# Kernel optimization log

Measured on AMD Instinct MI355X. Metric: run time of the kernel, lower is better.

## Reference

```python
import jax, jax.numpy as jnp
import numpy as np

B, N, P, PL = 8, 16, 128, 16
D, DS, DTR, DFF, EL = 128, 16, 8, 256, 2


def setup_inputs() -> dict:
    key = jax.random.key(0)
    ks = jax.random.split(key, 16)
    g = lambda i, shape, s=0.02: jax.random.normal(ks[i], shape, dtype=jnp.float32) * s
    A_init = jnp.broadcast_to(jnp.log(jnp.arange(1, DS + 1, dtype=jnp.float32)), (EL, 2, D, DS))
    return dict(
        x=jax.random.normal(ks[0], (B, N, P, PL), dtype=jnp.float32),
        view=jax.random.normal(ks[1], (B, 1, D), dtype=jnp.float32),
        wp_w=g(2, (D, PL)), wp_b=jnp.zeros((D,), jnp.float32),
        m_in_w=g(3, (EL, 2, 2 * D, D)),
        m_conv_w=g(4, (EL, 2, D, 2), 0.5), m_conv_b=jnp.zeros((EL, 2, D), jnp.float32),
        m_xproj_w=g(5, (EL, 2, DTR + 2 * DS, D)),
        m_dt_w=g(6, (EL, 2, D, DTR), 0.1), m_dt_b=jnp.full((EL, 2, D), -4.6, jnp.float32),
        m_Alog=jnp.array(A_init),
        m_D=jnp.ones((EL, 2, D), jnp.float32),
        m_out_w=g(7, (EL, 2, D, D)),
        ffn_w1=g(8, (EL, DFF, D)), ffn_b1=jnp.zeros((EL, DFF), jnp.float32),
        ffn_w2=g(9, (EL, D, DFF)), ffn_b2=jnp.zeros((EL, D), jnp.float32),
        ln1_g=jnp.ones((EL, D), jnp.float32), ln1_b=jnp.zeros((EL, D), jnp.float32),
        ln2_g=jnp.ones((EL, D), jnp.float32), ln2_b=jnp.zeros((EL, D), jnp.float32),
        lnf_g=jnp.ones((D,), jnp.float32), lnf_b=jnp.zeros((D,), jnp.float32),
    )


def _ln(x, g, b, eps=1e-5):
    m = x.mean(-1, keepdims=True)
    v = x.var(-1, keepdims=True)
    return (x - m) * jax.lax.rsqrt(v + eps) * g + b


def _mamba(u, in_w, conv_w, conv_b, xproj_w, dt_w, dt_b, A_log, Dp, out_w):
    # u: [b, L, d]; d_inner == d_model (expand=1), causal depthwise conv with kernel 2
    dtr, ds = dt_w.shape[1], A_log.shape[1]
    xz = u @ in_w.T                               # [b, L, 2d]
    xc, z = jnp.split(xz, 2, axis=-1)
    xp = jnp.pad(xc, ((0, 0), (1, 0), (0, 0)))    # left-pad (d_conv-1 = 1)
    xc = xp[:, :-1, :] * conv_w[:, 0] + xp[:, 1:, :] * conv_w[:, 1] + conv_b
    xc = jax.nn.silu(xc)
    dbc = xc @ xproj_w.T                          # [b, L, dtr + 2*ds]
    dt = jax.nn.softplus(dbc[..., :dtr] @ dt_w.T + dt_b)   # [b, L, d]
    Bm = dbc[..., dtr:dtr + ds]                   # [b, L, n]
    Cm = dbc[..., dtr + ds:]                      # [b, L, n]
    A = -jnp.exp(A_log)                           # [d, n]
    dA = jnp.exp(dt[..., None] * A)               # [b, L, d, n]
    dBx = dt[..., None] * Bm[:, :, None, :] * xc[..., None]  # [b, L, d, n]

    def step(h, ab):
        a, bx = ab
        h = a * h + bx
        return h, h

    h0 = jnp.zeros((u.shape[0], dt.shape[-1], ds), u.dtype)
    _, hs = jax.lax.scan(step, h0, (jnp.moveaxis(dA, 1, 0), jnp.moveaxis(dBx, 1, 0)))
    y = jnp.einsum('lbdn,bln->bld', hs, Cm)       # [b, L, d]
    y = y + xc * Dp
    y = y * jax.nn.silu(z)
    return y @ out_w.T


def _layer(u, pf, pr, w1, b1, w2, b2, g1, be1, g2, be2):
    fwd = _mamba(u, *pf)
    rev = _mamba(u[:, ::-1], *pr)[:, ::-1]
    u = u + fwd + rev
    xr = _ln(u, g1, be1)
    y = jax.nn.relu(xr @ w1.T + b1) @ w2.T + b2   # 1x1 conv FFN == pointwise linear
    return _ln(xr + y, g2, be2)


def reference(x, view, wp_w, wp_b, m_in_w, m_conv_w, m_conv_b, m_xproj_w, m_dt_w,
              m_dt_b, m_Alog, m_D, m_out_w, ffn_w1, ffn_b1, ffn_w2, ffn_b2,
              ln1_g, ln1_b, ln2_g, ln2_b, lnf_g, lnf_b):
    b, n, p, _ = x.shape
    u = x @ wp_w.T + wp_b                         # [b, n, p, d]
    d = u.shape[-1]
    u = u.reshape(b, n * p, d)
    u = jnp.concatenate([u, view], axis=1)        # [b, n*p+1, d]
    for l in range(m_in_w.shape[0]):
        pf = (m_in_w[l, 0], m_conv_w[l, 0], m_conv_b[l, 0], m_xproj_w[l, 0],
              m_dt_w[l, 0], m_dt_b[l, 0], m_Alog[l, 0], m_D[l, 0], m_out_w[l, 0])
        pr = (m_in_w[l, 1], m_conv_w[l, 1], m_conv_b[l, 1], m_xproj_w[l, 1],
              m_dt_w[l, 1], m_dt_b[l, 1], m_Alog[l, 1], m_D[l, 1], m_out_w[l, 1])
        u = _layer(u, pf, pr, ffn_w1[l], ffn_b1[l], ffn_w2[l], ffn_b2[l],
                   ln1_g[l], ln1_b[l], ln2_g[l], ln2_b[l])
    u = _ln(u, lnf_g, lnf_b)
    z = u[:, :-1, :].reshape(b, n, p, d)
    return z.transpose(0, 1, 3, 2)                # [b, n, d, p]
```

## Files before the change

### kernel.cpp

```cpp
#include <hip/hip_runtime.h>
#include <hip/hip_bf16.h>
#include <math.h>

#define DEV __device__ __forceinline__

constexpr int B  = 8,  N = 16, P = 128, PL = 16;
constexpr int D  = 128, DS = 16, DTR = 8, DFF = 256, EL = 2;
constexpr int L  = N * P + 1;
constexpr int BL = B * L;
constexpr int CT = 32;
constexpr int NC = (L + CT - 1) / CT;
constexpr int MT128 = (BL + 127) / 128;
constexpr int MT64  = (BL + 63) / 64;
constexpr int KS = 136;
constexpr int HS = 264;

using bf16x8 = __attribute__((ext_vector_type(8))) __bf16;
using f32x4  = __attribute__((ext_vector_type(4))) float;

DEV float sigmoidf_(float x) { return 1.0f / (1.0f + __expf(-x)); }

DEV float wsum(float v) {
#pragma unroll
  for (int m = 32; m; m >>= 1) v += __shfl_xor(v, m, 64);
  return v;
}

DEV void pow_tree(float r, float* pw) {
  float r2 = r * r;
  float r3 = r2 * r;
  float r4 = r2 * r2;
  float r8 = r4 * r4;
  float r12 = r8 * r4;
  pw[0] = r;       pw[1] = r2;      pw[2] = r3;      pw[3] = r4;
  pw[4] = r4 * r;  pw[5] = r4 * r2; pw[6] = r4 * r3; pw[7] = r8;
  pw[8] = r8 * r;  pw[9] = r8 * r2; pw[10] = r8 * r3; pw[11] = r12;
  pw[12] = r12 * r; pw[13] = r12 * r2; pw[14] = r12 * r3; pw[15] = r12 * r4;
}

DEV bool an_is_linear(const float* An) {
  bool ok = true;
#pragma unroll
  for (int n = 0; n < DS; ++n)
    ok = ok && (fabsf(An[n] + (float)(n + 1)) < 1e-3f * (n + 1));
  return ok;
}

__global__ __launch_bounds__(256) void k_prep(
    const float* __restrict__ in_w, const float* __restrict__ conv_w,
    const float* __restrict__ xproj, const float* __restrict__ out_w,
    const float* __restrict__ w1, const float* __restrict__ w2,
    __bf16* __restrict__ weff, __bf16* __restrict__ xpw_bf,
    __bf16* __restrict__ outw_bf, __bf16* __restrict__ w1_bf,
    __bf16* __restrict__ w2_bf)
{
  int g = blockIdx.x * 256 + threadIdx.x;
  if (g < 262144) {
    int l = g >> 17;
    int r = g & 131071;
    int dir = r >> 16;
    int r2 = r & 65535;
    int col = r2 >> 8;
    int kk = r2 & 255;
    int chunk = kk >> 7, k = kk & 127;
    int ld = l * 2 + dir;
    float v;
    if (col < 128) {
      v = in_w[((size_t)ld * 256 + col) * 128 + k] *
          conv_w[((size_t)ld * 128 + col) * 2 + chunk];
    } else {
      v = chunk ? in_w[((size_t)ld * 256 + col) * 128 + k] : 0.f;
    }
    weff[((size_t)ld * 256 + col) * 256 + chunk * 128 + k] = (__bf16)v;
    return;
  }
  g -= 262144;
  if (g < 20480) { xpw_bf[g] = (__bf16)xproj[g]; return; }
  g -= 20480;
  if (g < 65536) {
    int k = g & 127; int q = g >> 7; int n = q & 127; int q2 = q >> 7;
    int dir = q2 & 1; int l = q2 >> 1;
    outw_bf[((size_t)(l * 128 + n)) * 256 + dir * 128 + k] = (__bf16)out_w[g];
    return;
  }
  g -= 65536;
  if (g < 65536) { w1_bf[g] = (__bf16)w1[g]; return; }
  g -= 65536;
  if (g < 65536) { w2_bf[g] = (__bf16)w2[g]; return; }
}

__global__ __launch_bounds__(256) void k_embed(
    const float* __restrict__ x, const float* __restrict__ view,
    const float* __restrict__ wp_w, const float* __restrict__ wp_b,
    float* __restrict__ U, __bf16* __restrict__ Ubf)
{
  int g = blockIdx.x * 256 + threadIdx.x;
  if (g >= BL * D) return;
  int d = g & (D - 1);
  int row = g >> 7;
  int b = row / L, t = row % L;
  float acc;
  if (t < N * P) {
    const float* xr = x + ((size_t)b * N * P + t) * PL;
    acc = wp_b[d];
#pragma unroll
    for (int k = 0; k < PL; ++k) acc += xr[k] * wp_w[d * PL + k];
  } else {
    acc = view[b * D + d];
  }
  U[(size_t)row * D + d] = acc;
  Ubf[(size_t)row * D + d] = (__bf16)acc;
}

__global__ __launch_bounds__(256) void k_front(
    const __bf16* __restrict__ Ubf, const __bf16* __restrict__ Weff,
    const float* __restrict__ conv_b_l, const __bf16* __restrict__ xpw,
    const float* __restrict__ dt_w_l, const float* __restrict__ dt_b_l,
    __bf16* __restrict__ XCCbf, __bf16* __restrict__ Zbf,
    float* __restrict__ BCb, __bf16* __restrict__ DTbf)
{
  __shared__ short As[64 * KS];
  __shared__ short Ws[64 * KS];
  __shared__ float dbs[64][9];
  int bx = blockIdx.x;
  int rdir = bx / MT64;
  int tile = bx % MT64;
  bool isx = (blockIdx.y == 0);
  int tid = threadIdx.x;
  int m0 = tile * 64;
  const __bf16* Wb = Weff + (size_t)rdir * 256 * 256;
  int wave = tid >> 6, lane = tid & 63, lm = lane & 15, lq = lane >> 4;
  int rr0 = tid >> 4, gcol = tid & 15;

  int aoff[4];
  unsigned vmask = 0, smask = 0;
  int shif = rdir ? 128 : -128;
#pragma unroll
  for (int i = 0; i < 4; ++i) {
    int rr = rr0 + 16 * i;
    int m = m0 + rr;
    aoff[i] = 0;
    if (m < BL) {
      int b = m / L, s = m - b * L;
      int idx1 = rdir ? (L - 1 - s) : s;
      aoff[i] = (b * L + idx1) * 128 + gcol * 8;
      vmask |= 1u << i;
      if (s >= 1) smask |= 1u << i;
    }
  }

  f32x4 zero4 = {0.f, 0.f, 0.f, 0.f};
  f32x4 acc[8];
#pragma unroll
  for (int c = 0; c < 8; ++c) acc[c] = zero4;

  int kc0 = isx ? 0 : 1;
  int colx = isx ? 0 : 128;
  for (int kc = kc0; kc < 2; ++kc) {
    if (kc != kc0) __syncthreads();
#pragma unroll
    for (int i = 0; i < 4; ++i) {
      int rr = rr0 + 16 * i;
      int4 v = make_int4(0, 0, 0, 0);
      bool ok = (vmask >> i) & 1;
      if (kc == 0) ok = ok && ((smask >> i) & 1);
      if (ok) v = *(const int4*)(Ubf + aoff[i] + (kc == 0 ? shif : 0));
      *(int4*)&As[rr * KS + gcol * 8] = v;
    }
    for (int ch = 0; ch < 2; ++ch) {
      if (ch) __syncthreads();
#pragma unroll
      for (int i = 0; i < 4; ++i) {
        int rr = rr0 + 16 * i;
        int4 v = *(const int4*)(Wb + (size_t)(colx + ch * 64 + rr) * 256 + kc * 128 + gcol * 8);
        *(int4*)&Ws[rr * KS + gcol * 8] = v;
      }
      __syncthreads();
      for (int ks = 0; ks < 128; ks += 32) {
        bf16x8 af = *(const bf16x8*)&As[(wave * 16 + lm) * KS + ks + lq * 8];
#pragma unroll
        for (int c = 0; c < 4; ++c) {
          bf16x8 bfr = *(const bf16x8*)&Ws[(c * 16 + lm) * KS + ks + lq * 8];
          acc[ch * 4 + c] = __builtin_amdgcn_mfma_f32_16x16x32_bf16(af, bfr, acc[ch * 4 + c], 0, 0, 0);
        }
      }
    }
  }

  if (!isx) {
#pragma unroll
    for (int cg = 0; cg < 8; ++cg) {
      int col = cg * 16 + lm;
#pragma unroll
      for (int e = 0; e < 4; ++e) {
        int m = m0 + wave * 16 + lq * 4 + e;
        if (m < BL)
          Zbf[((size_t)rdir * BL + m) * 128 + col] = (__bf16)acc[cg][e];
      }
    }
    return;
  }

  __syncthreads();
#pragma unroll
  for (int cg = 0; cg < 8; ++cg) {
    int col = cg * 16 + lm;
    float cb = conv_b_l[rdir * 128 + col];
#pragma unroll
    for (int e = 0; e < 4; ++e) {
      int rl = wave * 16 + lq * 4 + e;
      int m = m0 + rl;
      float v = acc[cg][e] + cb;
      float o = v * sigmoidf_(v);
      __bf16 ob = (__bf16)o;
      if (m < BL) XCCbf[((size_t)rdir * BL + m) * 128 + col] = ob;
      As[rl * KS + col] = (short)__builtin_bit_cast(unsigned short, ob);
    }
  }
#pragma unroll
  for (int i = 0; i < 3; ++i) {
    int rr = rr0 + 16 * i;
    int4 v = make_int4(0, 0, 0, 0);
    if (rr < 40) v = *(const int4*)(xpw + ((size_t)rdir * 40 + rr) * 128 + gcol * 8);
    *(int4*)&Ws[rr * KS + gcol * 8] = v;
  }
  __syncthreads();
  f32x4 acc2[3];
#pragma unroll
  for (int c = 0; c < 3; ++c) acc2[c] = zero4;
  for (int ks = 0; ks < 128; ks += 32) {
    bf16x8 af = *(const bf16x8*)&As[(wave * 16 + lm) * KS + ks + lq * 8];
#pragma unroll
    for (int c = 0; c < 3; ++c) {
      bf16x8 bfr = *(const bf16x8*)&Ws[(c * 16 + lm) * KS + ks + lq * 8];
      acc2[c] = __builtin_amdgcn_mfma_f32_16x16x32_bf16(af, bfr, acc2[c], 0, 0, 0);
    }
  }
#pragma unroll
  for (int c = 0; c < 3; ++c) {
    int col = c * 16 + lm;
#pragma unroll
    for (int e = 0; e < 4; ++e) {
      int rl = wave * 16 + lq * 4 + e;
      int m = m0 + rl;
      float v = acc2[c][e];
      if (col < DTR) dbs[rl][col] = v;
      else if (col < DTR + 2 * DS && m < BL)
        BCb[((size_t)rdir * BL + m) * 32 + (col - DTR)] = v;
    }
  }
  __syncthreads();
  {
    int dloc = tid & 127;
    int rpar = tid >> 7;
    const float* dw = dt_w_l + ((size_t)rdir * 128 + dloc) * 8;
    float dwr[8];
#pragma unroll
    for (int j = 0; j < 8; ++j) dwr[j] = dw[j];
    float db = dt_b_l[rdir * 128 + dloc];
    for (int rr = rpar; rr < 64; rr += 2) {
      int m = m0 + rr;
      if (m >= BL) break;
      float a = db;
#pragma unroll
      for (int j = 0; j < 8; ++j) a = fmaf(dbs[rr][j], dwr[j], a);
      float dtv = (a > 20.f) ? a : log1pf(__expf(a));
      DTbf[((size_t)rdir * BL + m) * 128 + dloc] = (__bf16)dtv;
    }
  }
}

__global__ __launch_bounds__(128) void k_scanA(
    const __bf16* __restrict__ DTbf, const __bf16* __restrict__ XCCbf,
    const float* __restrict__ BCb, const float* __restrict__ Alog_l,
    float* __restrict__ HC, float* __restrict__ DTS)
{
  __shared__ float Bs[CT][DS];
  __shared__ __bf16 DTs[CT][128];
  __shared__ __bf16 XCs[CT][128];
  __shared__ float HT[128][DS + 1];
  int blk = blockIdx.x;
  int c  = blk % NC;
  int rb = blk / NC;
  int rdir = rb / B;
  int d = threadIdx.x;
  int s0 = c * CT;
  int cn = min(CT, L - s0);
  size_t rowbase = (size_t)rb * L + s0;
  for (int q = d; q < cn * DS; q += 128)
    Bs[q >> 4][q & 15] = BCb[(rowbase + (q >> 4)) * 32 + (q & 15)];
  for (int q = d; q < cn * 16; q += 128) {
    int row = q >> 4, c8 = (q & 15) * 8;
    *(int4*)&DTs[row][c8] = *(const int4*)(DTbf + (rowbase + row) * D + c8);
    *(int4*)&XCs[row][c8] = *(const int4*)(XCCbf + (rowbase + row) * D + c8);
  }
  float An[DS];
  const float* Ab = Alog_l + (size_t)rdir * D * DS + (size_t)d * DS;
#pragma unroll
  for (int n = 0; n < DS; ++n) An[n] = -__expf(Ab[n]);
  bool fast = an_is_linear(An);
  __syncthreads();
  float h[DS];
#pragma unroll
  for (int n = 0; n < DS; ++n) h[n] = 0.f;
  float dts = 0.f;
  if (fast) {
    for (int ss = 0; ss < cn; ++ss) {
      float dt = (float)DTs[ss][d];
      float xc = (float)XCs[ss][d];
      dts += dt;
      float e = dt * xc;
      float pw[DS];
      pow_tree(__expf(-dt), pw);
#pragma unroll
      for (int n = 0; n < DS; ++n)
        h[n] = fmaf(pw[n], h[n], e * Bs[ss][n]);
    }
  } else {
    for (int ss = 0; ss < cn; ++ss) {
      float dt = (float)DTs[ss][d];
      float xc = (float)XCs[ss][d];
      dts += dt;
      float e = dt * xc;
#pragma unroll
      for (int n = 0; n < DS; ++n)
        h[n] = __expf(dt * An[n]) * h[n] + e * Bs[ss][n];
    }
  }
  DTS[(size_t)blk * D + d] = dts;
#pragma unroll
  for (int n = 0; n < DS; ++n) HT[d][n] = h[n];
  __syncthreads();
  for (int q = d; q < D * DS; q += 128) {
    int n = q >> 7, dd = q & 127;
    HC[((size_t)blk * DS + n) * D + dd] = HT[dd][n];
  }
}

__global__ __launch_bounds__(128) void k_scanB(
    const float* __restrict__ HC, const float* __restrict__ DTS,
    const float* __restrict__ Alog_l, float* __restrict__ HIN)
{
  int rb = blockIdx.x >> 4;
  int n  = blockIdx.x & 15;
  int rdir = rb / B;
  int d = threadIdx.x;
  float An_v = -__expf(Alog_l[((size_t)rdir * D + d) * DS + n]);
  float hc[8], dts[8];
#pragma unroll
  for (int k = 0; k < 8; ++k) {
    int cc = (k < NC) ? k : NC - 1;
    hc[k]  = HC[((size_t)(rb * NC + cc) * DS + n) * D + d];
    dts[k] = DTS[((size_t)(rb * NC + cc)) * D + d];
  }
  float h = 0.f;
  for (int c = 0; c < NC; c += 8) {
#pragma unroll
    for (int k = 0; k < 8; ++k) {
      int cc = c + k;
      if (cc >= NC) break;
      HIN[((size_t)(rb * NC + cc) * DS + n) * D + d] = h;
      h = __expf(dts[k] * An_v) * h + hc[k];
      int cp = cc + 8 < NC ? cc + 8 : NC - 1;
      hc[k]  = HC[((size_t)(rb * NC + cp) * DS + n) * D + d];
      dts[k] = DTS[((size_t)(rb * NC + cp)) * D + d];
    }
  }
}

__global__ __launch_bounds__(128) void k_scanC(
    const __bf16* __restrict__ DTbf, const __bf16* __restrict__ XCCbf,
    const float* __restrict__ BCb, const __bf16* __restrict__ Zbf,
    const float* __restrict__ HIN, const float* __restrict__ Alog_l,
    const float* __restrict__ Dp_l, __bf16* __restrict__ YMbf)
{
  __shared__ float Bsm[CT][DS];
  __shared__ float Csm[CT][DS];
  __shared__ __bf16 DTs[CT][128];
  __shared__ __bf16 XCs[CT][128];
  __shared__ __bf16 Zs[CT][128];
  int blk = blockIdx.x;
  int c  = blk % NC;
  int rb = blk / NC;
  int rdir = rb / B;
  int b = rb % B;
  int d = threadIdx.x;
  int s0 = c * CT;
  int cn = min(CT, L - s0);
  size_t rowbase = (size_t)rb * L + s0;
  for (int q = d; q < cn * 2 * DS; q += 128) {
    int ss = q >> 5, j = q & 31;
    float vv = BCb[(rowbase + ss) * 32 + j];
    if (j < DS) Bsm[ss][j] = vv; else Csm[ss][j - DS] = vv;
  }
  for (int q = d; q < cn * 16; q += 128) {
    int row = q >> 4, c8 = (q & 15) * 8;
    *(int4*)&DTs[row][c8] = *(const int4*)(DTbf + (rowbase + row) * D + c8);
    *(int4*)&XCs[row][c8] = *(const int4*)(XCCbf + (rowbase + row) * D + c8);
    *(int4*)&Zs[row][c8]  = *(const int4*)(Zbf + (rowbase + row) * D + c8);
  }
  float An[DS];
  const float* Ab = Alog_l + (size_t)rdir * D * DS + (size_t)d * DS;
#pragma unroll
  for (int n = 0; n < DS; ++n) An[n] = -__expf(Ab[n]);
  bool fast = an_is_linear(An);
  float h[DS];
#pragma unroll
  for (int n = 0; n < DS; ++n)
    h[n] = HIN[((size_t)blk * DS + n) * D + d];
  float Dpv = Dp_l[rdir * D + d];
  __syncthreads();
  if (fast) {
    for (int ss = 0; ss < cn; ++ss) {
      float dt = (float)DTs[ss][d];
      float xc = (float)XCs[ss][d];
      float z  = (float)Zs[ss][d];
      float e = dt * xc;
      float pw[DS];
      pow_tree(__expf(-dt), pw);
      float y = xc * Dpv;
#pragma unroll
      for (int n = 0; n < DS; ++n) {
        h[n] = fmaf(pw[n], h[n], e * Bsm[ss][n]);
        y = fmaf(h[n], Csm[ss][n], y);
      }
      y *= z * sigmoidf_(z);
      int s = s0 + ss;
      int tt = rdir ? (L - 1 - s) : s;
      YMbf[((size_t)b * L + tt) * 256 + rdir * 128 + d] = (__bf16)y;
    }
  } else {
    for (int ss = 0; ss < cn; ++ss) {
      float dt = (float)DTs[ss][d];
      float xc = (float)XCs[ss][d];
      float z  = (float)Zs[ss][d];
      float e = dt * xc;
      float y = xc * Dpv;
#pragma unroll
      for (int n = 0; n < DS; ++n) {
        h[n] = __expf(dt * An[n]) * h[n] + e * Bsm[ss][n];
        y = fmaf(h[n], Csm[ss][n], y);
      }
      y *= z * sigmoidf_(z);
      int s = s0 + ss;
      int tt = rdir ? (L - 1 - s) : s;
      YMbf[((size_t)b * L + tt) * 256 + rdir * 128 + d] = (__bf16)y;
    }
  }
}

__global__ __launch_bounds__(256) void k_tail(
    const __bf16* __restrict__ YMbf, const __bf16* __restrict__ Wout,
    const float* __restrict__ g1, const float* __restrict__ be1,
    const __bf16* __restrict__ w1bf, const float* __restrict__ b1,
    const __bf16* __restrict__ w2bf, const float* __restrict__ b2,
    const float* __restrict__ g2, const float* __restrict__ be2,
    float* __restrict__ U, __bf16* __restrict__ Ubf,
    int last, const float* __restrict__ lnfg, const float* __restrict__ lnfb,
    float* __restrict__ outp)
{
  __shared__ short AX[64 * KS];
  __shared__ short BH[128 * KS];
  __shared__ short Ws[64 * KS];
  int m0 = blockIdx.x * 64;
  int tid = threadIdx.x;
  int wave = tid >> 6, lane = tid & 63, lm = lane & 15, lq = lane >> 4;
  int rr0 = tid >> 4, gcol = tid & 15;
  f32x4 zero4 = {0.f, 0.f, 0.f, 0.f};

  f32x4 acc[8];
#pragma unroll
  for (int c = 0; c < 8; ++c) acc[c] = zero4;
  for (int kc = 0; kc < 2; ++kc) {
    if (kc) __syncthreads();
    for (int q = tid; q < 64 * 16; q += 256) {
      int rr = q >> 4, g = q & 15;
      int m = m0 + rr;
      int4 v = make_int4(0, 0, 0, 0);
      if (m < BL) v = *(const int4*)(YMbf + (size_t)m * 256 + kc * 128 + g * 8);
      *(int4*)&AX[rr * KS + g * 8] = v;
    }
    for (int q = tid; q < 128 * 16; q += 256) {
      int rr = q >> 4, g = q & 15;
      int4 v = *(const int4*)(Wout + (size_t)rr * 256 + kc * 128 + g * 8);
      *(int4*)&BH[rr * KS + g * 8] = v;
    }
    __syncthreads();
    for (int ks = 0; ks < 128; ks += 32) {
      bf16x8 af = *(const bf16x8*)&AX[(wave * 16 + lm) * KS + ks + lq * 8];
#pragma unroll
      for (int c = 0; c < 8; ++c) {
        bf16x8 bfr = *(const bf16x8*)&BH[(c * 16 + lm) * KS + ks + lq * 8];
        acc[c] = __builtin_amdgcn_mfma_f32_16x16x32_bf16(af, bfr, acc[c], 0, 0, 0);
      }
    }
  }
  __syncthreads();

  {
    float g1c[8], be1c[8];
#pragma unroll
    for (int c = 0; c < 8; ++c) {
      int col = c * 16 + lm;
      g1c[c] = g1[col]; be1c[c] = be1[col];
    }
#pragma unroll
    for (int r = 0; r < 4; ++r) {
      int row = m0 + wave * 16 + lq * 4 + r;
      bool valid = row < BL;
      float os[8];
      float sum = 0.f;
#pragma unroll
      for (int c = 0; c < 8; ++c) {
        int col = c * 16 + lm;
        float uv = valid ? U[(size_t)row * 128 + col] : 0.f;
        os[c] = acc[c][r] + uv;
        sum += os[c];
      }
#pragma unroll
      for (int mm = 1; mm < 16; mm <<= 1) sum += __shfl_xor(sum, mm, 64);
      float mean = sum * (1.f / 128.f);
      float qv = 0.f;
#pragma unroll
      for (int c = 0; c < 8; ++c) { float dv = os[c] - mean; qv += dv * dv; }
#pragma unroll
      for (int mm = 1; mm < 16; mm <<= 1) qv += __shfl_xor(qv, mm, 64);
      float inv = rsqrtf(qv * (1.f / 128.f) + 1e-5f);
      int rl = wave * 16 + lq * 4 + r;
#pragma unroll
      for (int c = 0; c < 8; ++c) {
        int col = c * 16 + lm;
        float o = (os[c] - mean) * inv * g1c[c] + be1c[c];
        AX[rl * KS + col] = (short)__builtin_bit_cast(unsigned short, (__bf16)o);
      }
    }
  }

  for (int cc = 0; cc < 4; ++cc) {
    __syncthreads();
    for (int q = tid; q < 64 * 16; q += 256) {
      int rr = q >> 4, g = q & 15;
      int4 v = *(const int4*)(w1bf + (size_t)(cc * 64 + rr) * 128 + g * 8);
      *(int4*)&Ws[rr * KS + g * 8] = v;
    }
    __syncthreads();
    f32x4 a1[4];
#pragma unroll
    for (int c = 0; c < 4; ++c) a1[c] = zero4;
    for (int ks = 0; ks < 128; ks += 32) {
      bf16x8 af = *(const bf16x8*)&AX[(wave * 16 + lm) * KS + ks + lq * 8];
#pragma unroll
      for (int c = 0; c < 4; ++c) {
        bf16x8 bfr = *(const bf16x8*)&Ws[(c * 16 + lm) * KS + ks + lq * 8];
        a1[c] = __builtin_amdgcn_mfma_f32_16x16x32_bf16(af, bfr, a1[c], 0, 0, 0);
      }
    }
#pragma unroll
    for (int c = 0; c < 4; ++c) {
      int col = cc * 64 + c * 16 + lm;
      float bb = b1[col];
#pragma unroll
      for (int e = 0; e < 4; ++e) {
        int rl = wave * 16 + lq * 4 + e;
        float hv = fmaxf(a1[c][e] + bb, 0.f);
        BH[rl * HS + col] = (short)__builtin_bit_cast(unsigned short, (__bf16)hv);
      }
    }
  }

  f32x4 a2[2][4];
#pragma unroll
  for (int nc = 0; nc < 2; ++nc)
#pragma unroll
    for (int c = 0; c < 4; ++c) a2[nc][c] = zero4;
  for (int nc = 0; nc < 2; ++nc) {
    for (int kc = 0; kc < 2; ++kc) {
      __syncthreads();
      for (int q = tid; q < 64 * 16; q += 256) {
        int rr = q >> 4, g = q & 15;
        int4 v = *(const int4*)(w2bf + (size_t)(nc * 64 + rr) * 256 + kc * 128 + g * 8);
        *(int4*)&Ws[rr * KS + g * 8] = v;
      }
      __syncthreads();
      for (int ks = 0; ks < 128; ks += 32) {
        bf16x8 af = *(const bf16x8*)&BH[(wave * 16 + lm) * HS + kc * 128 + ks + lq * 8];
#pragma unroll
        for (int c = 0; c < 4; ++c) {
          bf16x8 bfr = *(const bf16x8*)&Ws[(c * 16 + lm) * KS + ks + lq * 8];
          a2[nc][c] = __builtin_amdgcn_mfma_f32_16x16x32_bf16(af, bfr, a2[nc][c], 0, 0, 0);
        }
      }
    }
  }
  {
    float b2c[8], g2c[8], be2c[8];
#pragma unroll
    for (int q = 0; q < 8; ++q) {
      int col = (q >> 2) * 64 + (q & 3) * 16 + lm;
      b2c[q] = b2[col]; g2c[q] = g2[col]; be2c[q] = be2[col];
    }
#pragma unroll
    for (int r = 0; r < 4; ++r) {
      int rl = wave * 16 + lq * 4 + r;
      int row = m0 + rl;
      bool valid = row < BL;
      float os[8];
      float sum = 0.f;
#pragma unroll
      for (int q = 0; q < 8; ++q) {
        int nc = q >> 2, c = q & 3;
        int col = nc * 64 + c * 16 + lm;
        __bf16 xb = __builtin_bit_cast(__bf16, (unsigned short)AX[rl * KS + col]);
        os[q] = a2[nc][c][r] + b2c[q] + (float)xb;
        sum += os[q];
      }
#pragma unroll
      for (int mm = 1; mm < 16; mm <<= 1) sum += __shfl_xor(sum, mm, 64);
      float mean = sum * (1.f / 128.f);
      float qv = 0.f;
#pragma unroll
      for (int q = 0; q < 8; ++q) { float dv = os[q] - mean; qv += dv * dv; }
#pragma unroll
      for (int mm = 1; mm < 16; mm <<= 1) qv += __shfl_xor(qv, mm, 64);
      float inv = rsqrtf(qv * (1.f / 128.f) + 1e-5f);
      float o[8];
#pragma unroll
      for (int q = 0; q < 8; ++q)
        o[q] = (os[q] - mean) * inv * g2c[q] + be2c[q];
      if (!last) {
        if (valid) {
#pragma unroll
          for (int q = 0; q < 8; ++q) {
            int col = (q >> 2) * 64 + (q & 3) * 16 + lm;
            U[(size_t)row * 128 + col] = o[q];
          }
        }
#pragma unroll
        for (int q = 0; q < 8; ++q) {
          int col = (q >> 2) * 64 + (q & 3) * 16 + lm;
          AX[rl * KS + col] = (short)__builtin_bit_cast(unsigned short, (__bf16)o[q]);
        }
      } else {
        float s2 = 0.f;
#pragma unroll
        for (int q = 0; q < 8; ++q) s2 += o[q];
#pragma unroll
        for (int mm = 1; mm < 16; mm <<= 1) s2 += __shfl_xor(s2, mm, 64);
        float mean2 = s2 * (1.f / 128.f);
        float qv2 = 0.f;
#pragma unroll
        for (int q = 0; q < 8; ++q) { float dv = o[q] - mean2; qv2 += dv * dv; }
#pragma unroll
        for (int mm = 1; mm < 16; mm <<= 1) qv2 += __shfl_xor(qv2, mm, 64);
        float inv2 = rsqrtf(qv2 * (1.f / 128.f) + 1e-5f);
        if (valid) {
          int bb = row / L;
          int t = row - bb * L;
          if (t < N * P) {
            int n = t >> 7, p = t & 127;
            size_t obase = (((size_t)bb * N + n) * D) * P + p;
#pragma unroll
            for (int q = 0; q < 8; ++q) {
              int col = (q >> 2) * 64 + (q & 3) * 16 + lm;
              float o2 = (o[q] - mean2) * inv2 * lnfg[col] + lnfb[col];
              outp[obase + (size_t)col * P] = o2;
            }
          }
        }
      }
    }
  }
  if (!last) {
    __syncthreads();
#pragma unroll
    for (int i = 0; i < 4; ++i) {
      int rr = rr0 + 16 * i;
      int m = m0 + rr;
      if (m < BL)
        *(int4*)(Ubf + (size_t)m * 128 + gcol * 8) = *(const int4*)&AX[rr * KS + gcol * 8];
    }
  }
}

extern "C" void kernel_launch(void* const* d_in, const int* in_sizes, int n_in,
                              void* d_out, int out_size, void* d_ws, size_t ws_size,
                              hipStream_t stream)
{
  (void)in_sizes; (void)n_in; (void)out_size; (void)ws_size;
  const float* x       = (const float*)d_in[0];
  const float* view    = (const float*)d_in[1];
  const float* wp_w    = (const float*)d_in[2];
  const float* wp_b    = (const float*)d_in[3];
  const float* m_in_w  = (const float*)d_in[4];
  const float* m_conv_w= (const float*)d_in[5];
  const float* m_conv_b= (const float*)d_in[6];
  const float* m_xproj = (const float*)d_in[7];
  const float* m_dt_w  = (const float*)d_in[8];
  const float* m_dt_b  = (const float*)d_in[9];
  const float* m_Alog  = (const float*)d_in[10];
  const float* m_Dp    = (const float*)d_in[11];
  const float* m_out_w = (const float*)d_in[12];
  const float* ffn_w1  = (const float*)d_in[13];
  const float* ffn_b1  = (const float*)d_in[14];
  const float* ffn_w2  = (const float*)d_in[15];
  const float* ffn_b2  = (const float*)d_in[16];
  const float* ln1_g   = (const float*)d_in[17];
  const float* ln1_b   = (const float*)d_in[18];
  const float* ln2_g   = (const float*)d_in[19];
  const float* ln2_b   = (const float*)d_in[20];
  const float* lnf_g   = (const float*)d_in[21];
  const float* lnf_b   = (const float*)d_in[22];
  float* out = (float*)d_out;

  float* W = (float*)d_ws;
  size_t off = 0;
  auto alloc = [&](size_t nfl) { float* p = W + off; off += (nfl + 3) & ~(size_t)3; return p; };
  float* U      = alloc((size_t)BL * D);
  float* Ubf_f  = alloc((size_t)BL * D / 2);
  float* XCC_f  = alloc((size_t)BL * D);
  float* Zbf_f  = alloc((size_t)BL * D);
  float* DT_f   = alloc((size_t)BL * D);
  float* BCb    = alloc((size_t)2 * BL * 2 * DS);
  float* YM_f   = alloc((size_t)BL * 256 / 2);
  float* HC     = alloc((size_t)2 * B * NC * D * DS);
  float* DTS    = alloc((size_t)2 * B * NC * D);
  float* HIN    = alloc((size_t)2 * B * NC * D * DS);
  float* weff_f = alloc(262144 / 2);
  float* xpw_f  = alloc(20480 / 2);
  float* outw_f = alloc(65536 / 2);
  float* w1_f   = alloc(65536 / 2);
  float* w2_f   = alloc(65536 / 2);

  __bf16* Ubf    = (__bf16*)Ubf_f;
  __bf16* XCCbf  = (__bf16*)XCC_f;
  __bf16* Zbf    = (__bf16*)Zbf_f;
  __bf16* DTbf   = (__bf16*)DT_f;
  __bf16* YMbf   = (__bf16*)YM_f;
  __bf16* weff   = (__bf16*)weff_f;
  __bf16* xpw_bf = (__bf16*)xpw_f;
  __bf16* outw_bf= (__bf16*)outw_f;
  __bf16* w1_bf  = (__bf16*)w1_f;
  __bf16* w2_bf  = (__bf16*)w2_f;

  k_prep<<<1872, 256, 0, stream>>>(m_in_w, m_conv_w, m_xproj, m_out_w, ffn_w1, ffn_w2,
                                   weff, xpw_bf, outw_bf, w1_bf, w2_bf);
  k_embed<<<(BL * D + 255) / 256, 256, 0, stream>>>(x, view, wp_w, wp_b, U, Ubf);

  for (int l = 0; l < EL; ++l) {
    const float* conv_b_l = m_conv_b + (size_t)l * 2 * D;
    const float* dt_w_l   = m_dt_w   + (size_t)l * 2 * D * DTR;
    const float* dt_b_l   = m_dt_b   + (size_t)l * 2 * D;
    const float* Alog_l   = m_Alog   + (size_t)l * 2 * D * DS;
    const float* Dp_l     = m_Dp     + (size_t)l * 2 * D;

    k_front <<<dim3(2 * MT64, 2), 256, 0, stream>>>(
        Ubf, weff + (size_t)l * 2 * 256 * 256, conv_b_l,
        xpw_bf + (size_t)l * 2 * 40 * 128, dt_w_l, dt_b_l,
        XCCbf, Zbf, BCb, DTbf);
    k_scanA <<<2 * B * NC, 128, 0, stream>>>(DTbf, XCCbf, BCb, Alog_l, HC, DTS);
    k_scanB <<<2 * B * 16, 128, 0, stream>>>(HC, DTS, Alog_l, HIN);
    k_scanC <<<2 * B * NC, 128, 0, stream>>>(DTbf, XCCbf, BCb, Zbf, HIN, Alog_l, Dp_l, YMbf);
    k_tail  <<<MT64, 256, 0, stream>>>(
        YMbf, outw_bf + (size_t)l * 128 * 256,
        ln1_g + l * D, ln1_b + l * D,
        w1_bf + (size_t)l * 256 * 128, ffn_b1 + l * DFF,
        w2_bf + (size_t)l * 128 * 256, ffn_b2 + l * D,
        ln2_g + l * D, ln2_b + l * D, U, Ubf,
        (l == EL - 1) ? 1 : 0, lnf_g, lnf_b, out);
  }
}
```

Baseline: 321.4 us.

## Halve k_tail row tile to 32 with 2x2 wave split and cross-wave LayerNorm

k_tail now processes 32 rows per block instead of 64, with the four waves arranged 2x2 so each wave owns 16 rows and half of the output columns. LayerNorm row statistics are combined across the two column-waves through a small shared-memory reduction buffer. Weight tiles are staged as full 128-row chunks, so there are fewer staging rounds per block. The grid doubles (about 514 blocks), which should fill more of the GPU's compute units, at the cost of more total weight reloads and extra barriers.

Measured after the change: 339.9 us. +5.8%, slower.

```diff
diff --git a/kernel.cpp b/kernel.cpp
--- a/kernel.cpp
+++ b/kernel.cpp
@@ -10,8 +10,8 @@
 constexpr int BL = B * L;
 constexpr int CT = 32;
 constexpr int NC = (L + CT - 1) / CT;
-constexpr int MT128 = (BL + 127) / 128;
 constexpr int MT64  = (BL + 63) / 64;
+constexpr int MT32  = (BL + 31) / 32;
 constexpr int KS = 136;
 constexpr int HS = 264;
 
@@ -19,12 +19,6 @@
 using f32x4  = __attribute__((ext_vector_type(4))) float;
 
 DEV float sigmoidf_(float x) { return 1.0f / (1.0f + __expf(-x)); }
-
-DEV float wsum(float v) {
-#pragma unroll
-  for (int m = 32; m; m >>= 1) v += __shfl_xor(v, m, 64);
-  return v;
-}
 
 DEV void pow_tree(float r, float* pw) {
   float r2 = r * r;
@@ -459,21 +453,22 @@
     int last, const float* __restrict__ lnfg, const float* __restrict__ lnfb,
     float* __restrict__ outp)
 {
-  __shared__ short AX[64 * KS];
-  __shared__ short BH[128 * KS];
-  __shared__ short Ws[64 * KS];
-  int m0 = blockIdx.x * 64;
+  __shared__ short AX[32 * KS];
+  __shared__ short HB[32 * HS];
+  __shared__ short Ws[128 * KS];
+  __shared__ float red[2][32][2];
+  int m0 = blockIdx.x * 32;
   int tid = threadIdx.x;
   int wave = tid >> 6, lane = tid & 63, lm = lane & 15, lq = lane >> 4;
-  int rr0 = tid >> 4, gcol = tid & 15;
+  int wm = wave >> 1, wn = wave & 1;
   f32x4 zero4 = {0.f, 0.f, 0.f, 0.f};
 
-  f32x4 acc[8];
-#pragma unroll
-  for (int c = 0; c < 8; ++c) acc[c] = zero4;
+  f32x4 acc[4];
+#pragma unroll
+  for (int c = 0; c < 4; ++c) acc[c] = zero4;
   for (int kc = 0; kc < 2; ++kc) {
     if (kc) __syncthreads();
-    for (int q = tid; q < 64 * 16; q += 256) {
+    for (int q = tid; q < 32 * 16; q += 256) {
       int rr = q >> 4, g = q & 15;
       int m = m0 + rr;
       int4 v = make_int4(0, 0, 0, 0);
@@ -483,14 +478,14 @@
     for (int q = tid; q < 128 * 16; q += 256) {
       int rr = q >> 4, g = q & 15;
       int4 v = *(const int4*)(Wout + (size_t)rr * 256 + kc * 128 + g * 8);
-      *(int4*)&BH[rr * KS + g * 8] = v;
+      *(int4*)&Ws[rr * KS + g * 8] = v;
     }
     __syncthreads();
     for (int ks = 0; ks < 128; ks += 32) {
-      bf16x8 af = *(const bf16x8*)&AX[(wave * 16 + lm) * KS + ks + lq * 8];
-#pragma unroll
-      for (int c = 0; c < 8; ++c) {
-        bf16x8 bfr = *(const bf16x8*)&BH[(c * 16 + lm) * KS + ks + lq * 8];
+      bf16x8 af = *(const bf16x8*)&AX[(wm * 16 + lm) * KS + ks + lq * 8];
+#pragma unroll
+      for (int c = 0; c < 4; ++c) {
+        bf16x8 bfr = *(const bf16x8*)&Ws[(wn * 64 + c * 16 + lm) * KS + ks + lq * 8];
         acc[c] = __builtin_amdgcn_mfma_f32_16x16x32_bf16(af, bfr, acc[c], 0, 0, 0);
       }
     }
@@ -498,49 +493,62 @@
   __syncthreads();
 
   {
-    float g1c[8], be1c[8];
-#pragma unroll
-    for (int c = 0; c < 8; ++c) {
-      int col = c * 16 + lm;
+    float g1c[4], be1c[4];
+#pragma unroll
+    for (int c = 0; c < 4; ++c) {
+      int col = wn * 64 + c * 16 + lm;
       g1c[c] = g1[col]; be1c[c] = be1[col];
     }
+    float os[4][4];
+    float mean[4];
 #pragma unroll
     for (int r = 0; r < 4; ++r) {
-      int row = m0 + wave * 16 + lq * 4 + r;
+      int rl = wm * 16 + lq * 4 + r;
+      int row = m0 + rl;
       bool valid = row < BL;
-      float os[8];
-      float sum = 0.f;
-#pragma unroll
-      for (int c = 0; c < 8; ++c) {
-        int col = c * 16 + lm;
+      float s = 0.f;
+#pragma unroll
+      for (int c = 0; c < 4; ++c) {
+        int col = wn * 64 + c * 16 + lm;
         float uv = valid ? U[(size_t)row * 128 + col] : 0.f;
-        os[c] = acc[c][r] + uv;
-        sum += os[c];
-      }
-#pragma unroll
-      for (int mm = 1; mm < 16; mm <<= 1) sum += __shfl_xor(sum, mm, 64);
-      float mean = sum * (1.f / 128.f);
+        os[r][c] = acc[c][r] + uv;
+        s += os[r][c];
+      }
+#pragma unroll
+      for (int mm = 1; mm < 16; mm <<= 1) s += __shfl_xor(s, mm, 64);
+      if (lm == 0) red[0][rl][wn] = s;
+    }
+    __syncthreads();
+#pragma unroll
+    for (int r = 0; r < 4; ++r) {
+      int rl = wm * 16 + lq * 4 + r;
+      mean[r] = (red[0][rl][0] + red[0][rl][1]) * (1.f / 128.f);
       float qv = 0.f;
 #pragma unroll
-      for (int c = 0; c < 8; ++c) { float dv = os[c] - mean; qv += dv * dv; }
+      for (int c = 0; c < 4; ++c) { float dv = os[r][c] - mean[r]; qv += dv * dv; }
 #pragma unroll
       for (int mm = 1; mm < 16; mm <<= 1) qv += __shfl_xor(qv, mm, 64);
-      float inv = rsqrtf(qv * (1.f / 128.f) + 1e-5f);
-      int rl = wave * 16 + lq * 4 + r;
-#pragma unroll
-      for (int c = 0; c < 8; ++c) {
-        int col = c * 16 + lm;
-        float o = (os[c] - mean) * inv * g1c[c] + be1c[c];
+      if (lm == 0) red[1][rl][wn] = qv;
+    }
+    __syncthreads();
+#pragma unroll
+    for (int r = 0; r < 4; ++r) {
+      int rl = wm * 16 + lq * 4 + r;
+      float inv = rsqrtf((red[1][rl][0] + red[1][rl][1]) * (1.f / 128.f) + 1e-5f);
+#pragma unroll
+      for (int c = 0; c < 4; ++c) {
+        int col = wn * 64 + c * 16 + lm;
+        float o = (os[r][c] - mean[r]) * inv * g1c[c] + be1c[c];
         AX[rl * KS + col] = (short)__builtin_bit_cast(unsigned short, (__bf16)o);
       }
     }
   }
 
-  for (int cc = 0; cc < 4; ++cc) {
-    __syncthreads();
-    for (int q = tid; q < 64 * 16; q += 256) {
+  for (int t = 0; t < 2; ++t) {
+    if (t) __syncthreads();
+    for (int q = tid; q < 128 * 16; q += 256) {
       int rr = q >> 4, g = q & 15;
-      int4 v = *(const int4*)(w1bf + (size_t)(cc * 64 + rr) * 128 + g * 8);
+      int4 v = *(const int4*)(w1bf + (size_t)(t * 128 + rr) * 128 + g * 8);
       *(int4*)&Ws[rr * KS + g * 8] = v;
     }
     __syncthreads();
@@ -548,121 +556,152 @@
 #pragma unroll
     for (int c = 0; c < 4; ++c) a1[c] = zero4;
     for (int ks = 0; ks < 128; ks += 32) {
-      bf16x8 af = *(const bf16x8*)&AX[(wave * 16 + lm) * KS + ks + lq * 8];
+      bf16x8 af = *(const bf16x8*)&AX[(wm * 16 + lm) * KS + ks + lq * 8];
 #pragma unroll
       for (int c = 0; c < 4; ++c) {
-        bf16x8 bfr = *(const bf16x8*)&Ws[(c * 16 + lm) * KS + ks + lq * 8];
+        bf16x8 bfr = *(const bf16x8*)&Ws[(wn * 64 + c * 16 + lm) * KS + ks + lq * 8];
         a1[c] = __builtin_amdgcn_mfma_f32_16x16x32_bf16(af, bfr, a1[c], 0, 0, 0);
       }
     }
 #pragma unroll
     for (int c = 0; c < 4; ++c) {
-      int col = cc * 64 + c * 16 + lm;
+      int col = t * 128 + wn * 64 + c * 16 + lm;
       float bb = b1[col];
 #pragma unroll
       for (int e = 0; e < 4; ++e) {
-        int rl = wave * 16 + lq * 4 + e;
+        int rl = wm * 16 + lq * 4 + e;
         float hv = fmaxf(a1[c][e] + bb, 0.f);
-        BH[rl * HS + col] = (short)__builtin_bit_cast(unsigned short, (__bf16)hv);
-      }
-    }
-  }
-
-  f32x4 a2[2][4];
-#pragma unroll
-  for (int nc = 0; nc < 2; ++nc)
-#pragma unroll
-    for (int c = 0; c < 4; ++c) a2[nc][c] = zero4;
-  for (int nc = 0; nc < 2; ++nc) {
-    for (int kc = 0; kc < 2; ++kc) {
-      __syncthreads();
-      for (int q = tid; q < 64 * 16; q += 256) {
-        int rr = q >> 4, g = q & 15;
-        int4 v = *(const int4*)(w2bf + (size_t)(nc * 64 + rr) * 256 + kc * 128 + g * 8);
-        *(int4*)&Ws[rr * KS + g * 8] = v;
-      }
-      __syncthreads();
-      for (int ks = 0; ks < 128; ks += 32) {
-        bf16x8 af = *(const bf16x8*)&BH[(wave * 16 + lm) * HS + kc * 128 + ks + lq * 8];
-#pragma unroll
-        for (int c = 0; c < 4; ++c) {
-          bf16x8 bfr = *(const bf16x8*)&Ws[(c * 16 + lm) * KS + ks + lq * 8];
-          a2[nc][c] = __builtin_amdgcn_mfma_f32_16x16x32_bf16(af, bfr, a2[nc][c], 0, 0, 0);
-        }
-      }
-    }
-  }
+        HB[rl * HS + col] = (short)__builtin_bit_cast(unsigned short, (__bf16)hv);
+      }
+    }
+  }
+
+  f32x4 a2[4];
+#pragma unroll
+  for (int c = 0; c < 4; ++c) a2[c] = zero4;
+  for (int kc = 0; kc < 2; ++kc) {
+    __syncthreads();
+    for (int q = tid; q < 128 * 16; q += 256) {
+      int rr = q >> 4, g = q & 15;
+      int4 v = *(const int4*)(w2bf + (size_t)rr * 256 + kc * 128 + g * 8);
+      *(int4*)&Ws[rr * KS + g * 8] = v;
+    }
+    __syncthreads();
+    for (int ks = 0; ks < 128; ks += 32) {
+      bf16x8 af = *(const bf16x8*)&HB[(wm * 16 + lm) * HS + kc * 128 + ks + lq * 8];
+#pragma unroll
+      for (int c = 0; c < 4; ++c) {
+        bf16x8 bfr = *(const bf16x8*)&Ws[(wn * 64 + c * 16 + lm) * KS + ks + lq * 8];
+        a2[c] = __builtin_amdgcn_mfma_f32_16x16x32_bf16(af, bfr, a2[c], 0, 0, 0);
+      }
+    }
+  }
+  __syncthreads();
+
   {
-    float b2c[8], g2c[8], be2c[8];
-#pragma unroll
-    for (int q = 0; q < 8; ++q) {
-      int col = (q >> 2) * 64 + (q & 3) * 16 + lm;
-      b2c[q] = b2[col]; g2c[q] = g2[col]; be2c[q] = be2[col];
-    }
+    float b2c[4], g2c[4], be2c[4];
+#pragma unroll
+    for (int c = 0; c < 4; ++c) {
+      int col = wn * 64 + c * 16 + lm;
+      b2c[c] = b2[col]; g2c[c] = g2[col]; be2c[c] = be2[col];
+    }
+    float os[4][4];
+    float mean[4];
 #pragma unroll
     for (int r = 0; r < 4; ++r) {
-      int rl = wave * 16 + lq * 4 + r;
-      int row = m0 + rl;
-      bool valid = row < BL;
-      float os[8];
-      float sum = 0.f;
-#pragma unroll
-      for (int q = 0; q < 8; ++q) {
-        int nc = q >> 2, c = q & 3;
-        int col = nc * 64 + c * 16 + lm;
+      int rl = wm * 16 + lq * 4 + r;
+      float s = 0.f;
+#pragma unroll
+      for (int c = 0; c < 4; ++c) {
+        int col = wn * 64 + c * 16 + lm;
         __bf16 xb = __builtin_bit_cast(__bf16, (unsigned short)AX[rl * KS + col]);
-        os[q] = a2[nc][c][r] + b2c[q] + (float)xb;
-        sum += os[q];
-      }
-#pragma unroll
-      for (int mm = 1; mm < 16; mm <<= 1) sum += __shfl_xor(sum, mm, 64);
-      float mean = sum * (1.f / 128.f);
+        os[r][c] = a2[c][r] + b2c[c] + (float)xb;
+        s += os[r][c];
+      }
+#pragma unroll
+      for (int mm = 1; mm < 16; mm <<= 1) s += __shfl_xor(s, mm, 64);
+      if (lm == 0) red[0][rl][wn] = s;
+    }
+    __syncthreads();
+#pragma unroll
+    for (int r = 0; r < 4; ++r) {
+      int rl = wm * 16 + lq * 4 + r;
+      mean[r] = (red[0][rl][0] + red[0][rl][1]) * (1.f / 128.f);
       float qv = 0.f;
 #pragma unroll
-      for (int q = 0; q < 8; ++q) { float dv = os[q] - mean; qv += dv * dv; }
+      for (int c = 0; c < 4; ++c) { float dv = os[r][c] - mean[r]; qv += dv * dv; }
 #pragma unroll
       for (int mm = 1; mm < 16; mm <<= 1) qv += __shfl_xor(qv, mm, 64);
-      float inv = rsqrtf(qv * (1.f / 128.f) + 1e-5f);
-      float o[8];
-#pragma unroll
-      for (int q = 0; q < 8; ++q)
-        o[q] = (os[q] - mean) * inv * g2c[q] + be2c[q];
-      if (!last) {
-        if (valid) {
-#pragma unroll
-          for (int q = 0; q < 8; ++q) {
-            int col = (q >> 2) * 64 + (q & 3) * 16 + lm;
-            U[(size_t)row * 128 + col] = o[q];
+      if (lm == 0) red[1][rl][wn] = qv;
+    }
+    __syncthreads();
+    float o[4][4];
+#pragma unroll
+    for (int r = 0; r < 4; ++r) {
+      int rl = wm * 16 + lq * 4 + r;
+      float inv = rsqrtf((red[1][rl][0] + red[1][rl][1]) * (1.f / 128.f) + 1e-5f);
+#pragma unroll
+      for (int c = 0; c < 4; ++c)
+        o[r][c] = (os[r][c] - mean[r]) * inv * g2c[c] + be2c[c];
+    }
+    if (!last) {
+#pragma unroll
+      for (int r = 0; r < 4; ++r) {
+        int rl = wm * 16 + lq * 4 + r;
+        int row = m0 + rl;
+        if (row < BL) {
+#pragma unroll
+          for (int c = 0; c < 4; ++c) {
+            int col = wn * 64 + c * 16 + lm;
+            U[(size_t)row * 128 + col] = o[r][c];
           }
         }
 #pragma unroll
-        for (int q = 0; q < 8; ++q) {
-          int col = (q >> 2) * 64 + (q & 3) * 16 + lm;
-          AX[rl * KS + col] = (short)__builtin_bit_cast(unsigned short, (__bf16)o[q]);
+        for (int c = 0; c < 4; ++c) {
+          int col = wn * 64 + c * 16 + lm;
+          AX[rl * KS + col] = (short)__builtin_bit_cast(unsigned short, (__bf16)o[r][c]);
         }
-      } else {
+      }
+    } else {
+      float m2[4];
+#pragma unroll
+      for (int r = 0; r < 4; ++r) {
+        int rl = wm * 16 + lq * 4 + r;
         float s2 = 0.f;
 #pragma unroll
-        for (int q = 0; q < 8; ++q) s2 += o[q];
+        for (int c = 0; c < 4; ++c) s2 += o[r][c];
 #pragma unroll
         for (int mm = 1; mm < 16; mm <<= 1) s2 += __shfl_xor(s2, mm, 64);
-        float mean2 = s2 * (1.f / 128.f);
-        float qv2 = 0.f;
-#pragma unroll
-        for (int q = 0; q < 8; ++q) { float dv = o[q] - mean2; qv2 += dv * dv; }
-#pragma unroll
-        for (int mm = 1; mm < 16; mm <<= 1) qv2 += __shfl_xor(qv2, mm, 64);
-        float inv2 = rsqrtf(qv2 * (1.f / 128.f) + 1e-5f);
-        if (valid) {
+        if (lm == 0) red[0][rl][wn] = s2;
+      }
+      __syncthreads();
+#pragma unroll
+      for (int r = 0; r < 4; ++r) {
+        int rl = wm * 16 + lq * 4 + r;
+        m2[r] = (red[0][rl][0] + red[0][rl][1]) * (1.f / 128.f);
+        float q2 = 0.f;
+#pragma unroll
+        for (int c = 0; c < 4; ++c) { float dv = o[r][c] - m2[r]; q2 += dv * dv; }
+#pragma unroll
+        for (int mm = 1; mm < 16; mm <<= 1) q2 += __shfl_xor(q2, mm, 64);
+        if (lm == 0) red[1][rl][wn] = q2;
+      }
+      __syncthreads();
+#pragma unroll
+      for (int r = 0; r < 4; ++r) {
+        int rl = wm * 16 + lq * 4 + r;
+        int row = m0 + rl;
+        float i2 = rsqrtf((red[1][rl][0] + red[1][rl][1]) * (1.f / 128.f) + 1e-5f);
+        if (row < BL) {
           int bb = row / L;
           int t = row - bb * L;
           if (t < N * P) {
             int n = t >> 7, p = t & 127;
             size_t obase = (((size_t)bb * N + n) * D) * P + p;
 #pragma unroll
-            for (int q = 0; q < 8; ++q) {
-              int col = (q >> 2) * 64 + (q & 3) * 16 + lm;
-              float o2 = (o[q] - mean2) * inv2 * lnfg[col] + lnfb[col];
+            for (int c = 0; c < 4; ++c) {
+              int col = wn * 64 + c * 16 + lm;
+              float o2 = (o[r][c] - m2[r]) * i2 * lnfg[col] + lnfb[col];
               outp[obase + (size_t)col * P] = o2;
             }
           }
@@ -672,8 +711,9 @@
   }
   if (!last) {
     __syncthreads();
-#pragma unroll
-    for (int i = 0; i < 4; ++i) {
+    int rr0 = tid >> 4, gcol = tid & 15;
+#pragma unroll
+    for (int i = 0; i < 2; ++i) {
       int rr = rr0 + 16 * i;
       int m = m0 + rr;
       if (m < BL)
@@ -760,7 +800,7 @@
     k_scanA <<<2 * B * NC, 128, 0, stream>>>(DTbf, XCCbf, BCb, Alog_l, HC, DTS);
     k_scanB <<<2 * B * 16, 128, 0, stream>>>(HC, DTS, Alog_l, HIN);
     k_scanC <<<2 * B * NC, 128, 0, stream>>>(DTbf, XCCbf, BCb, Zbf, HIN, Alog_l, Dp_l, YMbf);
-    k_tail  <<<MT64, 256, 0, stream>>>(
+    k_tail  <<<MT32, 256, 0, stream>>>(
         YMbf, outw_bf + (size_t)l * 128 * 256,
         ln1_g + l * D, ln1_b + l * D,
         w1_bf + (size_t)l * 256 * 128, ffn_b1 + l * DFF,
```
